# Performance work log

Measured on AMD Instinct MI355X. Metric: run time of the kernel, lower is better.

## Reference

```python
import jax, jax.numpy as jnp
import numpy as np

NUM_EMBEDDINGS = 1024
EMBEDDING_DIM = 64
BETA = 0.25


def setup_inputs() -> dict:
    key = jax.random.key(0)
    k1, k2 = jax.random.split(key)
    z = jax.random.normal(k1, (64, 32, 32, EMBEDDING_DIM), dtype=jnp.float32)
    emb = jax.random.uniform(
        k2, (NUM_EMBEDDINGS, EMBEDDING_DIM), dtype=jnp.float32,
        minval=-1.0 / NUM_EMBEDDINGS, maxval=1.0 / NUM_EMBEDDINGS)
    return {"z": z, "emb": emb}


def reference(z, emb):
    zf = z.reshape(-1, EMBEDDING_DIM)                      # [N, D]
    # squared L2 distances via ||z||^2 - 2 z.e + ||e||^2  -> [N, K]
    distances = (jnp.sum(zf * zf, axis=1, keepdims=True)
                 - 2.0 * jnp.matmul(zf, emb.T)
                 + jnp.sum(emb * emb, axis=1))
    encoding_indices = jnp.argmin(distances, axis=1)       # [N]
    quantized = emb[encoding_indices].reshape(z.shape)     # [B, H, W, D]
    commitment_loss = BETA * jnp.mean((jax.lax.stop_gradient(quantized) - z) ** 2)
    codebook_loss = jnp.mean((quantized - jax.lax.stop_gradient(z)) ** 2)
    loss = commitment_loss + codebook_loss
    # straight-through estimator
    quantized = z + jax.lax.stop_gradient(quantized - z)
    return (quantized, loss)
```

## Files before the change

### kernel.cpp

```cpp
#include <hip/hip_runtime.h>
#include <stdint.h>

#define N_ROWS 65536
#define K_CODES 1024
#define D 64
#define OUT_ELEMS 4194304
#define LOSS_SCALE (1.25f / 4194304.0f)
#define ROWS_PER_BLOCK 128
#define GRID_DIST (N_ROWS / ROWS_PER_BLOCK)

typedef short short8 __attribute__((ext_vector_type(8)));
typedef float f32x4 __attribute__((ext_vector_type(4)));

__device__ __forceinline__ unsigned short f2bf(float f) {
    unsigned int u = __float_as_uint(f);
    return (unsigned short)((u + 0x7fffu + ((u >> 16) & 1u)) >> 16);
}

#define GLOAD_LDS16(g, l)                                                          \
    __builtin_amdgcn_global_load_lds((const __attribute__((address_space(1))) void*)(g), \
                                     (__attribute__((address_space(3))) void*)(l), 16, 0, 0)

#define ECH (K_CODES * D / 8)
__global__ __launch_bounds__(256) void prep_kernel(const float* __restrict__ emb,
                                                   unsigned short* __restrict__ ebm2,
                                                   float* __restrict__ e2) {
    int t = blockIdx.x * 256 + threadIdx.x;
    if (t < ECH) {
        const float4* s = (const float4*)emb;
        float4 a = s[2 * t], b = s[2 * t + 1];
        uint4 o;
        o.x = f2bf(-2.f * a.x) | ((unsigned int)f2bf(-2.f * a.y) << 16);
        o.y = f2bf(-2.f * a.z) | ((unsigned int)f2bf(-2.f * a.w) << 16);
        o.z = f2bf(-2.f * b.x) | ((unsigned int)f2bf(-2.f * b.y) << 16);
        o.w = f2bf(-2.f * b.z) | ((unsigned int)f2bf(-2.f * b.w) << 16);
        ((uint4*)ebm2)[t] = o;
    } else if (t < ECH + K_CODES) {
        int k = t - ECH;
        const float4* e4 = (const float4*)emb;
        float s = 0.f;
#pragma unroll
        for (int i = 0; i < 16; i++) {
            float4 v = e4[k * 16 + i];
            s += v.x * v.x + v.y * v.y + v.z * v.z + v.w * v.w;
        }
        e2[k] = s;
    }
}

__global__ __launch_bounds__(256, 2) void dist_fused_kernel(
        const float* __restrict__ z, const unsigned short* __restrict__ ebm2,
        const float* __restrict__ e2, const float* __restrict__ emb,
        float* __restrict__ out, float* __restrict__ partials) {
    __shared__ __align__(16) char smem[65536];
    const int tid = threadIdx.x;
    const int wave = tid >> 6, lane = tid & 63;
    const int n = lane & 15, q = lane >> 4, nb = n & 7;
    const int block_row0 = blockIdx.x * ROWS_PER_BLOCK;

    short8 b[2][2];
#pragma unroll
    for (int rs = 0; rs < 2; rs++) {
        const float* zr = z + (size_t)(block_row0 + wave * 32 + rs * 16 + n) * D + q * 8;
        float4 f0 = *(const float4*)(zr);
        float4 f1 = *(const float4*)(zr + 4);
        float4 f2 = *(const float4*)(zr + 32);
        float4 f3 = *(const float4*)(zr + 36);
        short8 lo, hi;
        lo[0] = f2bf(f0.x); lo[1] = f2bf(f0.y); lo[2] = f2bf(f0.z); lo[3] = f2bf(f0.w);
        lo[4] = f2bf(f1.x); lo[5] = f2bf(f1.y); lo[6] = f2bf(f1.z); lo[7] = f2bf(f1.w);
        hi[0] = f2bf(f2.x); hi[1] = f2bf(f2.y); hi[2] = f2bf(f2.z); hi[3] = f2bf(f2.w);
        hi[4] = f2bf(f3.x); hi[5] = f2bf(f3.y); hi[6] = f2bf(f3.z); hi[7] = f2bf(f3.w);
        b[rs][0] = lo; b[rs][1] = hi;
    }

    auto stage = [&](int c) {
        const int bufoff = (c & 1) << 15;
        const uint4* gsrc = (const uint4*)ebm2;
#pragma unroll
        for (int r = 0; r < 8; r++) {
            int S = c * 2048 + r * 256 + tid;
            int P = (S & ~7) | ((S & 7) ^ ((S >> 3) & 7));
            char* l = smem + bufoff + (r * 256 + (tid & ~63)) * 16;
            GLOAD_LDS16(gsrc + P, l);
        }
    };

    f32x4 Ea = *(const f32x4*)(e2 + q * 4);
    f32x4 Eb = *(const f32x4*)(e2 + 16 + q * 4);
    const int base0 = n * 128 + ((q ^ nb) << 4);
    const int base1 = n * 128 + (((4 | q) ^ nb) << 4);

    float bestd[2] = {INFINITY, INFINITY};
    int bestk[2] = {0, 0};

    stage(0);
    __syncthreads();
    for (int c = 0; c < 4; c++) {
        if (c < 3) stage(c + 1);
        const char* buf = smem + ((c & 1) << 15);
#pragma unroll
        for (int tl = 0; tl < 16; tl++) {
            const int t = c * 16 + tl;
            short8 a0 = *(const short8*)(buf + tl * 2048 + base0);
            short8 a1 = *(const short8*)(buf + tl * 2048 + base1);
            f32x4 E = (tl & 1) ? Eb : Ea;
            f32x4 acc0 = E, acc1 = E;
            acc0 = __builtin_amdgcn_mfma_f32_16x16x32_bf16(a0, b[0][0], acc0, 0, 0, 0);
            acc0 = __builtin_amdgcn_mfma_f32_16x16x32_bf16(a1, b[0][1], acc0, 0, 0, 0);
            acc1 = __builtin_amdgcn_mfma_f32_16x16x32_bf16(a0, b[1][0], acc1, 0, 0, 0);
            acc1 = __builtin_amdgcn_mfma_f32_16x16x32_bf16(a1, b[1][1], acc1, 0, 0, 0);
            int tp = (t + 2 > 63) ? 63 : (t + 2);
            f32x4 En = *(const f32x4*)(e2 + tp * 16 + q * 4);
            if (tl & 1) Eb = En; else Ea = En;
#pragma unroll
            for (int r = 0; r < 4; r++) {
                float d0 = acc0[r];
                if (d0 < bestd[0]) { bestd[0] = d0; bestk[0] = t * 16 + q * 4 + r; }
                float d1 = acc1[r];
                if (d1 < bestd[1]) { bestd[1] = d1; bestk[1] = t * 16 + q * 4 + r; }
            }
        }
        __syncthreads();
    }

    int* sh_idx = (int*)smem;
    float* ps = (float*)(smem + 512);
#pragma unroll
    for (int rs = 0; rs < 2; rs++) {
        unsigned int db = __float_as_uint(bestd[rs]);
        db = (db & 0x80000000u) ? ~db : (db | 0x80000000u);
        unsigned long long key = ((unsigned long long)db << 32) | (unsigned int)bestk[rs];
        unsigned long long o = __shfl_xor(key, 16, 64); key = o < key ? o : key;
        o = __shfl_xor(key, 32, 64); key = o < key ? o : key;
        if (q == 0) sh_idx[wave * 32 + rs * 16 + n] = (int)(key & 0xFFFFFFFFu);
    }
    __syncthreads();

    float ssum = 0.f;
    const float4* z4 = (const float4*)z;
    float4* o4 = (float4*)out;
#pragma unroll
    for (int it = 0; it < 8; it++) {
        int cidx = it * 256 + tid;
        int lrow = cidx >> 4, d4 = cidx & 15;
        int k = sh_idx[lrow];
        size_t gi = (size_t)block_row0 * 16 + cidx;
        float4 qv = ((const float4*)emb)[k * 16 + d4];
        float4 zv = z4[gi];
        o4[gi] = qv;
        float dx = qv.x - zv.x, dy = qv.y - zv.y, dz = qv.z - zv.z, dw = qv.w - zv.w;
        ssum += dx * dx + dy * dy + dz * dz + dw * dw;
    }
#pragma unroll
    for (int off = 32; off > 0; off >>= 1)
        ssum += __shfl_down(ssum, off, 64);
    if (lane == 0) ps[wave] = ssum;
    __syncthreads();
    if (tid == 0) partials[blockIdx.x] = ps[0] + ps[1] + ps[2] + ps[3];
}

__global__ __launch_bounds__(256) void loss_kernel(const float* __restrict__ partials,
                                                   float* __restrict__ loss) {
    float s = partials[threadIdx.x] + partials[threadIdx.x + 256];
#pragma unroll
    for (int off = 32; off > 0; off >>= 1)
        s += __shfl_down(s, off, 64);
    __shared__ float ps[4];
    int wave = threadIdx.x >> 6, lane = threadIdx.x & 63;
    if (lane == 0) ps[wave] = s;
    __syncthreads();
    if (threadIdx.x == 0) loss[0] = (ps[0] + ps[1] + ps[2] + ps[3]) * LOSS_SCALE;
}

extern "C" void kernel_launch(void* const* d_in, const int* in_sizes, int n_in,
                              void* d_out, int out_size, void* d_ws, size_t ws_size,
                              hipStream_t stream) {
    const float* z = (const float*)d_in[0];
    const float* emb = (const float*)d_in[1];
    float* out = (float*)d_out;
    float* loss = out + OUT_ELEMS;

    char* ws = (char*)d_ws;
    float* e2 = (float*)ws;
    unsigned short* ebm2 = (unsigned short*)(ws + 4096);
    float* partials = (float*)(ws + 4096 + 131072 + 8192);

    prep_kernel<<<(ECH + K_CODES + 255) / 256, 256, 0, stream>>>(emb, ebm2, e2);
    dist_fused_kernel<<<GRID_DIST, 256, 0, stream>>>(z, ebm2, e2, emb, out, partials);
    loss_kernel<<<1, 256, 0, stream>>>(partials, loss);
}
```

Before: 90.53 us.

## Process 64 rows per wave and derive loss from best distance plus z norm

Each wave now handles 64 rows (four 16-row MFMA tiles) against each staged codebook chunk, doubling rows per block so every LDS codebook load is reused by twice as many rows. The loss is computed as the sum of the minimal bf16-MFMA distance plus a per-row fp32 ||z||^2, which removes the second read of z in the epilogue. The output gather now uses lane shuffles instead of an LDS index table. The trade-off is half as many blocks (256, one per CU with only 4 waves), higher register pressure, and a loss value that inherits bf16 rounding error from the distance computation.

```diff
diff --git a/kernel.cpp b/kernel.cpp
--- a/kernel.cpp
+++ b/kernel.cpp
@@ -6,7 +6,7 @@
 #define D 64
 #define OUT_ELEMS 4194304
 #define LOSS_SCALE (1.25f / 4194304.0f)
-#define ROWS_PER_BLOCK 128
+#define ROWS_PER_BLOCK 256
 #define GRID_DIST (N_ROWS / ROWS_PER_BLOCK)
 
 typedef short short8 __attribute__((ext_vector_type(8)));
@@ -48,7 +48,7 @@
     }
 }
 
-__global__ __launch_bounds__(256, 2) void dist_fused_kernel(
+__global__ __launch_bounds__(256) void dist_fused_kernel(
         const float* __restrict__ z, const unsigned short* __restrict__ ebm2,
         const float* __restrict__ e2, const float* __restrict__ emb,
         float* __restrict__ out, float* __restrict__ partials) {
@@ -56,23 +56,7 @@
     const int tid = threadIdx.x;
     const int wave = tid >> 6, lane = tid & 63;
     const int n = lane & 15, q = lane >> 4, nb = n & 7;
-    const int block_row0 = blockIdx.x * ROWS_PER_BLOCK;
-
-    short8 b[2][2];
-#pragma unroll
-    for (int rs = 0; rs < 2; rs++) {
-        const float* zr = z + (size_t)(block_row0 + wave * 32 + rs * 16 + n) * D + q * 8;
-        float4 f0 = *(const float4*)(zr);
-        float4 f1 = *(const float4*)(zr + 4);
-        float4 f2 = *(const float4*)(zr + 32);
-        float4 f3 = *(const float4*)(zr + 36);
-        short8 lo, hi;
-        lo[0] = f2bf(f0.x); lo[1] = f2bf(f0.y); lo[2] = f2bf(f0.z); lo[3] = f2bf(f0.w);
-        lo[4] = f2bf(f1.x); lo[5] = f2bf(f1.y); lo[6] = f2bf(f1.z); lo[7] = f2bf(f1.w);
-        hi[0] = f2bf(f2.x); hi[1] = f2bf(f2.y); hi[2] = f2bf(f2.z); hi[3] = f2bf(f2.w);
-        hi[4] = f2bf(f3.x); hi[5] = f2bf(f3.y); hi[6] = f2bf(f3.z); hi[7] = f2bf(f3.w);
-        b[rs][0] = lo; b[rs][1] = hi;
-    }
+    const int wave_row0 = blockIdx.x * ROWS_PER_BLOCK + wave * 64;
 
     auto stage = [&](int c) {
         const int bufoff = (c & 1) << 15;
@@ -85,16 +69,37 @@
             GLOAD_LDS16(gsrc + P, l);
         }
     };
+    stage(0);
+
+    short8 b[4][2];
+    float z2p[4];
+#pragma unroll
+    for (int rs = 0; rs < 4; rs++) {
+        const float* zr = z + (size_t)(wave_row0 + rs * 16 + n) * D + q * 8;
+        float4 f0 = *(const float4*)(zr);
+        float4 f1 = *(const float4*)(zr + 4);
+        float4 f2 = *(const float4*)(zr + 32);
+        float4 f3 = *(const float4*)(zr + 36);
+        z2p[rs] = f0.x*f0.x + f0.y*f0.y + f0.z*f0.z + f0.w*f0.w
+                + f1.x*f1.x + f1.y*f1.y + f1.z*f1.z + f1.w*f1.w
+                + f2.x*f2.x + f2.y*f2.y + f2.z*f2.z + f2.w*f2.w
+                + f3.x*f3.x + f3.y*f3.y + f3.z*f3.z + f3.w*f3.w;
+        short8 lo, hi;
+        lo[0] = f2bf(f0.x); lo[1] = f2bf(f0.y); lo[2] = f2bf(f0.z); lo[3] = f2bf(f0.w);
+        lo[4] = f2bf(f1.x); lo[5] = f2bf(f1.y); lo[6] = f2bf(f1.z); lo[7] = f2bf(f1.w);
+        hi[0] = f2bf(f2.x); hi[1] = f2bf(f2.y); hi[2] = f2bf(f2.z); hi[3] = f2bf(f2.w);
+        hi[4] = f2bf(f3.x); hi[5] = f2bf(f3.y); hi[6] = f2bf(f3.z); hi[7] = f2bf(f3.w);
+        b[rs][0] = lo; b[rs][1] = hi;
+    }
 
     f32x4 Ea = *(const f32x4*)(e2 + q * 4);
     f32x4 Eb = *(const f32x4*)(e2 + 16 + q * 4);
     const int base0 = n * 128 + ((q ^ nb) << 4);
     const int base1 = n * 128 + (((4 | q) ^ nb) << 4);
 
-    float bestd[2] = {INFINITY, INFINITY};
-    int bestk[2] = {0, 0};
+    float bestd[4] = {INFINITY, INFINITY, INFINITY, INFINITY};
+    int bestk[4] = {0, 0, 0, 0};
 
-    stage(0);
     __syncthreads();
     for (int c = 0; c < 4; c++) {
         if (c < 3) stage(c + 1);
@@ -105,64 +110,66 @@
             short8 a0 = *(const short8*)(buf + tl * 2048 + base0);
             short8 a1 = *(const short8*)(buf + tl * 2048 + base1);
             f32x4 E = (tl & 1) ? Eb : Ea;
-            f32x4 acc0 = E, acc1 = E;
-            acc0 = __builtin_amdgcn_mfma_f32_16x16x32_bf16(a0, b[0][0], acc0, 0, 0, 0);
-            acc0 = __builtin_amdgcn_mfma_f32_16x16x32_bf16(a1, b[0][1], acc0, 0, 0, 0);
-            acc1 = __builtin_amdgcn_mfma_f32_16x16x32_bf16(a0, b[1][0], acc1, 0, 0, 0);
-            acc1 = __builtin_amdgcn_mfma_f32_16x16x32_bf16(a1, b[1][1], acc1, 0, 0, 0);
+            f32x4 acc[4];
+#pragma unroll
+            for (int rs = 0; rs < 4; rs++) {
+                f32x4 a = E;
+                a = __builtin_amdgcn_mfma_f32_16x16x32_bf16(a0, b[rs][0], a, 0, 0, 0);
+                a = __builtin_amdgcn_mfma_f32_16x16x32_bf16(a1, b[rs][1], a, 0, 0, 0);
+                acc[rs] = a;
+            }
             int tp = (t + 2 > 63) ? 63 : (t + 2);
             f32x4 En = *(const f32x4*)(e2 + tp * 16 + q * 4);
             if (tl & 1) Eb = En; else Ea = En;
 #pragma unroll
-            for (int r = 0; r < 4; r++) {
-                float d0 = acc0[r];
-                if (d0 < bestd[0]) { bestd[0] = d0; bestk[0] = t * 16 + q * 4 + r; }
-                float d1 = acc1[r];
-                if (d1 < bestd[1]) { bestd[1] = d1; bestk[1] = t * 16 + q * 4 + r; }
-            }
+            for (int rs = 0; rs < 4; rs++)
+#pragma unroll
+                for (int r = 0; r < 4; r++) {
+                    float d = acc[rs][r];
+                    if (d < bestd[rs]) { bestd[rs] = d; bestk[rs] = t * 16 + q * 4 + r; }
+                }
         }
         __syncthreads();
     }
 
-    int* sh_idx = (int*)smem;
-    float* ps = (float*)(smem + 512);
+    float lossl = 0.f;
+    int bidx[4];
 #pragma unroll
-    for (int rs = 0; rs < 2; rs++) {
+    for (int rs = 0; rs < 4; rs++) {
         unsigned int db = __float_as_uint(bestd[rs]);
         db = (db & 0x80000000u) ? ~db : (db | 0x80000000u);
         unsigned long long key = ((unsigned long long)db << 32) | (unsigned int)bestk[rs];
         unsigned long long o = __shfl_xor(key, 16, 64); key = o < key ? o : key;
         o = __shfl_xor(key, 32, 64); key = o < key ? o : key;
-        if (q == 0) sh_idx[wave * 32 + rs * 16 + n] = (int)(key & 0xFFFFFFFFu);
+        bidx[rs] = (int)(key & 0xFFFFFFFFu);
+        unsigned int eu = (unsigned int)(key >> 32);
+        float bd = __uint_as_float((eu & 0x80000000u) ? (eu & 0x7FFFFFFFu) : ~eu);
+        float z2r = z2p[rs];
+        z2r += __shfl_xor(z2r, 16, 64);
+        z2r += __shfl_xor(z2r, 32, 64);
+        lossl += bd + z2r;
     }
-    __syncthreads();
 
-    float ssum = 0.f;
-    const float4* z4 = (const float4*)z;
-    float4* o4 = (float4*)out;
+    const float4* emb4 = (const float4*)emb;
+    float4* o4 = (float4*)out + (size_t)wave_row0 * 16;
 #pragma unroll
-    for (int it = 0; it < 8; it++) {
-        int cidx = it * 256 + tid;
-        int lrow = cidx >> 4, d4 = cidx & 15;
-        int k = sh_idx[lrow];
-        size_t gi = (size_t)block_row0 * 16 + cidx;
-        float4 qv = ((const float4*)emb)[k * 16 + d4];
-        float4 zv = z4[gi];
-        o4[gi] = qv;
-        float dx = qv.x - zv.x, dy = qv.y - zv.y, dz = qv.z - zv.z, dw = qv.w - zv.w;
-        ssum += dx * dx + dy * dy + dz * dz + dw * dw;
+    for (int it = 0; it < 16; it++) {
+        int k = __shfl(bidx[it >> 2], (it * 4 + q) & 15, 64);
+        o4[it * 64 + lane] = emb4[k * 16 + n];
     }
+
 #pragma unroll
     for (int off = 32; off > 0; off >>= 1)
-        ssum += __shfl_down(ssum, off, 64);
-    if (lane == 0) ps[wave] = ssum;
+        lossl += __shfl_down(lossl, off, 64);
+    float* ps = (float*)smem;
+    if (lane == 0) ps[wave] = lossl;
     __syncthreads();
-    if (tid == 0) partials[blockIdx.x] = ps[0] + ps[1] + ps[2] + ps[3];
+    if (tid == 0) partials[blockIdx.x] = 0.25f * (ps[0] + ps[1] + ps[2] + ps[3]);
 }
 
 __global__ __launch_bounds__(256) void loss_kernel(const float* __restrict__ partials,
                                                    float* __restrict__ loss) {
-    float s = partials[threadIdx.x] + partials[threadIdx.x + 256];
+    float s = partials[threadIdx.x];
 #pragma unroll
     for (int off = 32; off > 0; off >>= 1)
         s += __shfl_down(s, off, 64);
```

After: 92.94 us. 1.03x slower.
